# Performance work log

Measured on AMD Instinct MI355X. Metric: run time of the kernel, lower is better.

Reference implementation:

```python
import jax, jax.numpy as jnp
import numpy as np

TOP_K = 8
NUM_EXPERTS = 256
N_GROUP = 8
TOPK_GROUP = 4
SCALE = 2.5
RENORMALIZE = True
TOKENS = 131072


def setup_inputs() -> dict:
    key = jax.random.key(0)
    k1, k2 = jax.random.split(key)
    router_logits = jax.random.normal(k1, (TOKENS, NUM_EXPERTS), dtype=jnp.float32)
    expert_bias = jax.random.normal(k2, (NUM_EXPERTS,), dtype=jnp.float32) * 0.1
    return {"router_logits": router_logits, "expert_bias": expert_bias}


def _group_limited_topk(biased):
    # biased: [T, E]
    T = biased.shape[0]
    epg = NUM_EXPERTS // N_GROUP  # experts per group
    grouped = biased.reshape(T, N_GROUP, epg)
    # group score = sum of top-2 expert scores in each group
    top2_vals, _ = jax.lax.top_k(grouped, 2)
    group_scores = top2_vals.sum(axis=-1)  # [T, G]
    _, group_idx = jax.lax.top_k(group_scores, TOPK_GROUP)  # [T, Kg]
    group_mask = jnp.zeros((T, N_GROUP), dtype=bool).at[
        jnp.arange(T)[:, None], group_idx
    ].set(True)
    score_mask = jnp.repeat(group_mask, epg, axis=-1)  # [T, E]
    masked = jnp.where(score_mask, biased, -jnp.inf)
    _, topk_ids = jax.lax.top_k(masked, TOP_K)  # [T, K]
    return topk_ids


def reference(router_logits, expert_bias):
    scores = jax.nn.sigmoid(router_logits.astype(jnp.float32)).astype(router_logits.dtype)
    topk_ids = _group_limited_topk(scores + expert_bias)
    topk_weights = jnp.take_along_axis(scores, topk_ids, axis=-1)  # [T, K]
    if RENORMALIZE and TOP_K > 1:
        topk_weights = topk_weights / (topk_weights.sum(axis=-1, keepdims=True) + 1e-20)
    topk_weights = topk_weights * SCALE
    return topk_weights, topk_ids
```

## Files before the change

kernel.cpp:

```cpp
#include <hip/hip_runtime.h>
#include <math.h>


#define SWZF(x, mask) __int_as_float(__builtin_amdgcn_ds_swizzle(__float_as_int(x), (((mask) << 10) | 0x1F)))
#define SWZI(x, mask) __builtin_amdgcn_ds_swizzle((x), (((mask) << 10) | 0x1F))

__global__ __launch_bounds__(256) void router_topk_kernel(
    const float* __restrict__ logits,
    const float* __restrict__ bias,
    float* __restrict__ out_w,
    float* __restrict__ out_id,
    int T)
{
    const float NEGINF = -__builtin_inff();
    const int tid = threadIdx.x;
    const int s = tid & 7;
    const int token = blockIdx.x * 32 + (tid >> 3);
    if (token >= T) return;

    const float* row = logits + (size_t)token * 256 + s * 32;
    const float* brw = bias + s * 32;

    float v[8][4];
    int   ix[8][4];

    #pragma unroll
    for (int c = 0; c < 8; ++c) {
        float4 l = ((const float4*)row)[c];
        float4 b = ((const float4*)brw)[c];
        #pragma unroll
        for (int k = 0; k < 4; ++k) {
            float x = (&l.x)[k];
            v[c][k] = 1.0f / (1.0f + expf(-x)) + (&b.x)[k];
            ix[c][k] = s * 32 + c * 4 + k;
        }
    }

    float t1 = NEGINF, t2 = NEGINF;
    #pragma unroll
    for (int c = 0; c < 8; ++c) {
        #pragma unroll
        for (int k = 0; k < 4; ++k) {
            float val = v[c][k];
            t2 = fmaxf(t2, fminf(t1, val));
            t1 = fmaxf(t1, val);
        }
    }
    const float gs = t1 + t2;

    int rank = 0;
    #define RANKSTEP(m, hb) { \
        float gj = SWZF(gs, m); \
        rank += (gj > gs || (gj == gs && (s & (hb)))) ? 1 : 0; }
    RANKSTEP(1, 1) RANKSTEP(2, 2) RANKSTEP(3, 2)
    RANKSTEP(4, 4) RANKSTEP(5, 4) RANKSTEP(6, 4) RANKSTEP(7, 4)
    #undef RANKSTEP
    const bool selected = rank < 4;

    #pragma unroll
    for (int c = 0; c < 8; ++c) {
        #pragma unroll
        for (int k = 0; k < 4; ++k)
            v[c][k] = selected ? v[c][k] : NEGINF;
    }

    #pragma unroll
    for (int c = 0; c < 8; ++c) {
        #define CE(a,b) { \
            bool sw = (v[c][a] < v[c][b]) || (v[c][a] == v[c][b] && ix[c][a] > ix[c][b]); \
            float tv = sw ? v[c][b] : v[c][a]; \
            float uv = sw ? v[c][a] : v[c][b]; \
            int   ti = sw ? ix[c][b] : ix[c][a]; \
            int   ui = sw ? ix[c][a] : ix[c][b]; \
            v[c][a] = tv; v[c][b] = uv; ix[c][a] = ti; ix[c][b] = ui; }
        CE(0,1) CE(2,3) CE(0,2) CE(1,3) CE(1,2)
        #undef CE
    }

    float keepV = 0.0f; int keepI = 0;
    const int sbase8 = s << 3;
    #pragma unroll
    for (int r = 0; r < 8; ++r) {
        #define PICK(av, ai, bv, bi, rv, ri) { \
            bool t = ((bv) > (av)); \
            rv = t ? (bv) : (av); ri = t ? (bi) : (ai); }
        float w0v, w1v, w2v, w3v, x0v, x1v, bv;
        int   w0i, w1i, w2i, w3i, x0i, x1i, bi;
        PICK(v[0][0], ix[0][0], v[1][0], ix[1][0], w0v, w0i)
        PICK(v[2][0], ix[2][0], v[3][0], ix[3][0], w1v, w1i)
        PICK(v[4][0], ix[4][0], v[5][0], ix[5][0], w2v, w2i)
        PICK(v[6][0], ix[6][0], v[7][0], ix[7][0], w3v, w3i)
        PICK(w0v, w0i, w1v, w1i, x0v, x0i)
        PICK(w2v, w2i, w3v, w3i, x1v, x1i)
        PICK(x0v, x0i, x1v, x1i, bv, bi)
        #undef PICK
        #define BFLY(m) { \
            float ov = SWZF(bv, m); int oi = SWZI(bi, m); \
            bool t = (ov > bv) || (ov == bv && oi < bi); \
            bv = t ? ov : bv; bi = t ? oi : bi; }
        BFLY(1) BFLY(2) BFLY(4)
        #undef BFLY
        if (s == r) { keepV = bv; keepI = bi; }
        const int d = (bi >> 2) - sbase8;
        #pragma unroll
        for (int c = 0; c < 8; ++c) {
            bool hit = (d == c);
            v[c][0]  = hit ? v[c][1]  : v[c][0];
            ix[c][0] = hit ? ix[c][1] : ix[c][0];
            v[c][1]  = hit ? v[c][2]  : v[c][1];
            ix[c][1] = hit ? ix[c][2] : ix[c][1];
            v[c][2]  = hit ? v[c][3]  : v[c][2];
            ix[c][2] = hit ? ix[c][3] : ix[c][2];
            v[c][3]  = hit ? NEGINF   : v[c][3];
        }
    }

    float w = keepV - bias[keepI];
    float sum = w;
    sum += SWZF(sum, 1);
    sum += SWZF(sum, 2);
    sum += SWZF(sum, 4);
    w = w / (sum + 1e-20f) * 2.5f;

    out_w[(size_t)token * 8 + s]  = w;
    out_id[(size_t)token * 8 + s] = (float)keepI;
}

extern "C" void kernel_launch(void* const* d_in, const int* in_sizes, int n_in,
                              void* d_out, int out_size, void* d_ws, size_t ws_size,
                              hipStream_t stream) {
    const float* logits = (const float*)d_in[0];
    const float* bias   = (const float*)d_in[1];
    const int E = in_sizes[1];
    const int T = in_sizes[0] / E;
    float* out_w  = (float*)d_out;
    float* out_id = out_w + (size_t)T * 8;
    const int blocks = (T + 31) / 32;
    router_topk_kernel<<<blocks, 256, 0, stream>>>(logits, bias, out_w, out_id, T);
}
```

Before: 210.2 us.

## Use fast approximate sigmoid with margin check and exact-recompute fallback

Computes the sigmoid with hardware exp2 and rcp approximations instead of the exact expf and division, then checks whether the group-selection or top-k decisions sit within small error margins. If any decision is close to a tie, the token is recomputed with the exact sigmoid and reselected. This aims to cut the transcendental arithmetic cost while keeping results identical to the exact path. The cost is an extra ninth selection round plus margin reductions, and divergent fallback work for tokens that trip the check.

```diff
diff --git a/kernel.cpp b/kernel.cpp
--- a/kernel.cpp
+++ b/kernel.cpp
@@ -13,6 +13,8 @@
     int T)
 {
     const float NEGINF = -__builtin_inff();
+    const float EM = 4e-6f;
+    const float GM = 1.2e-5f;
     const int tid = threadIdx.x;
     const int s = tid & 7;
     const int token = blockIdx.x * 32 + (tid >> 3);
@@ -24,95 +26,127 @@
     float v[8][4];
     int   ix[8][4];
 
-    #pragma unroll
-    for (int c = 0; c < 8; ++c) {
-        float4 l = ((const float4*)row)[c];
-        float4 b = ((const float4*)brw)[c];
+    auto compute = [&](int exact) {
         #pragma unroll
-        for (int k = 0; k < 4; ++k) {
-            float x = (&l.x)[k];
-            v[c][k] = 1.0f / (1.0f + expf(-x)) + (&b.x)[k];
-            ix[c][k] = s * 32 + c * 4 + k;
+        for (int c = 0; c < 8; ++c) {
+            float4 l = ((const float4*)row)[c];
+            float4 b = ((const float4*)brw)[c];
+            #pragma unroll
+            for (int k = 0; k < 4; ++k) {
+                float x = (&l.x)[k];
+                float sg;
+                if (exact) {
+                    sg = 1.0f / (1.0f + expf(-x));
+                } else {
+                    float e = __builtin_amdgcn_exp2f(x * -1.4426950408889634f);
+                    sg = __builtin_amdgcn_rcpf(1.0f + e);
+                }
+                v[c][k] = sg + (&b.x)[k];
+            }
         }
-    }
-
-    float t1 = NEGINF, t2 = NEGINF;
-    #pragma unroll
-    for (int c = 0; c < 8; ++c) {
-        #pragma unroll
-        for (int k = 0; k < 4; ++k) {
-            float val = v[c][k];
-            t2 = fmaxf(t2, fminf(t1, val));
-            t1 = fmaxf(t1, val);
-        }
-    }
-    const float gs = t1 + t2;
-
-    int rank = 0;
-    #define RANKSTEP(m, hb) { \
-        float gj = SWZF(gs, m); \
-        rank += (gj > gs || (gj == gs && (s & (hb)))) ? 1 : 0; }
-    RANKSTEP(1, 1) RANKSTEP(2, 2) RANKSTEP(3, 2)
-    RANKSTEP(4, 4) RANKSTEP(5, 4) RANKSTEP(6, 4) RANKSTEP(7, 4)
-    #undef RANKSTEP
-    const bool selected = rank < 4;
-
-    #pragma unroll
-    for (int c = 0; c < 8; ++c) {
-        #pragma unroll
-        for (int k = 0; k < 4; ++k)
-            v[c][k] = selected ? v[c][k] : NEGINF;
-    }
-
-    #pragma unroll
-    for (int c = 0; c < 8; ++c) {
-        #define CE(a,b) { \
-            bool sw = (v[c][a] < v[c][b]) || (v[c][a] == v[c][b] && ix[c][a] > ix[c][b]); \
-            float tv = sw ? v[c][b] : v[c][a]; \
-            float uv = sw ? v[c][a] : v[c][b]; \
-            int   ti = sw ? ix[c][b] : ix[c][a]; \
-            int   ui = sw ? ix[c][a] : ix[c][b]; \
-            v[c][a] = tv; v[c][b] = uv; ix[c][a] = ti; ix[c][b] = ui; }
-        CE(0,1) CE(2,3) CE(0,2) CE(1,3) CE(1,2)
-        #undef CE
-    }
+    };
 
     float keepV = 0.0f; int keepI = 0;
     const int sbase8 = s << 3;
-    #pragma unroll
-    for (int r = 0; r < 8; ++r) {
-        #define PICK(av, ai, bv, bi, rv, ri) { \
-            bool t = ((bv) > (av)); \
-            rv = t ? (bv) : (av); ri = t ? (bi) : (ai); }
-        float w0v, w1v, w2v, w3v, x0v, x1v, bv;
-        int   w0i, w1i, w2i, w3i, x0i, x1i, bi;
-        PICK(v[0][0], ix[0][0], v[1][0], ix[1][0], w0v, w0i)
-        PICK(v[2][0], ix[2][0], v[3][0], ix[3][0], w1v, w1i)
-        PICK(v[4][0], ix[4][0], v[5][0], ix[5][0], w2v, w2i)
-        PICK(v[6][0], ix[6][0], v[7][0], ix[7][0], w3v, w3i)
-        PICK(w0v, w0i, w1v, w1i, x0v, x0i)
-        PICK(w2v, w2i, w3v, w3i, x1v, x1i)
-        PICK(x0v, x0i, x1v, x1i, bv, bi)
-        #undef PICK
-        #define BFLY(m) { \
-            float ov = SWZF(bv, m); int oi = SWZI(bi, m); \
-            bool t = (ov > bv) || (ov == bv && oi < bi); \
-            bv = t ? ov : bv; bi = t ? oi : bi; }
-        BFLY(1) BFLY(2) BFLY(4)
-        #undef BFLY
-        if (s == r) { keepV = bv; keepI = bi; }
-        const int d = (bi >> 2) - sbase8;
+
+    auto select = [&](bool& flag) {
+        #pragma unroll
+        for (int c = 0; c < 8; ++c)
+            #pragma unroll
+            for (int k = 0; k < 4; ++k)
+                ix[c][k] = s * 32 + c * 4 + k;
+
+        float t1 = NEGINF, t2 = NEGINF;
         #pragma unroll
         for (int c = 0; c < 8; ++c) {
-            bool hit = (d == c);
-            v[c][0]  = hit ? v[c][1]  : v[c][0];
-            ix[c][0] = hit ? ix[c][1] : ix[c][0];
-            v[c][1]  = hit ? v[c][2]  : v[c][1];
-            ix[c][1] = hit ? ix[c][2] : ix[c][1];
-            v[c][2]  = hit ? v[c][3]  : v[c][2];
-            ix[c][2] = hit ? ix[c][3] : ix[c][2];
-            v[c][3]  = hit ? NEGINF   : v[c][3];
+            #pragma unroll
+            for (int k = 0; k < 4; ++k) {
+                float val = v[c][k];
+                t2 = fmaxf(t2, fminf(t1, val));
+                t1 = fmaxf(t1, val);
+            }
         }
+        const float gs = t1 + t2;
+
+        int rank = 0;
+        #define RANKSTEP(m, hb) { \
+            float gj = SWZF(gs, m); \
+            rank += (gj > gs || (gj == gs && (s & (hb)))) ? 1 : 0; }
+        RANKSTEP(1, 1) RANKSTEP(2, 2) RANKSTEP(3, 2)
+        RANKSTEP(4, 4) RANKSTEP(5, 4) RANKSTEP(6, 4) RANKSTEP(7, 4)
+        #undef RANKSTEP
+        const bool selected = rank < 4;
+
+        float a  = selected ? NEGINF : gs;
+        float nb = selected ? -gs : NEGINF;
+        a  = fmaxf(a,  SWZF(a, 1));  nb = fmaxf(nb, SWZF(nb, 1));
+        a  = fmaxf(a,  SWZF(a, 2));  nb = fmaxf(nb, SWZF(nb, 2));
+        a  = fmaxf(a,  SWZF(a, 4));  nb = fmaxf(nb, SWZF(nb, 4));
+        flag = ((-nb) - a) < GM;
+
+        #pragma unroll
+        for (int c = 0; c < 8; ++c) {
+            #define CE(x,y) { \
+                bool sw = (v[c][x] < v[c][y]) || (v[c][x] == v[c][y] && ix[c][x] > ix[c][y]); \
+                float tv = sw ? v[c][y] : v[c][x]; \
+                float uv = sw ? v[c][x] : v[c][y]; \
+                int   ti = sw ? ix[c][y] : ix[c][x]; \
+                int   ui = sw ? ix[c][x] : ix[c][y]; \
+                v[c][x] = tv; v[c][y] = uv; ix[c][x] = ti; ix[c][y] = ui; }
+            CE(0,1) CE(2,3) CE(0,2) CE(1,3) CE(1,2)
+            #undef CE
+        }
+
+        float prev = 0.0f;
+        #pragma unroll
+        for (int r = 0; r < 9; ++r) {
+            #define PICK(av, ai, bv_, bi_, rv, ri) { \
+                bool t = ((bv_) > (av)); \
+                rv = t ? (bv_) : (av); ri = t ? (bi_) : (ai); }
+            float w0v, w1v, w2v, w3v, x0v, x1v, bv;
+            int   w0i, w1i, w2i, w3i, x0i, x1i, bi;
+            PICK(v[0][0], ix[0][0], v[1][0], ix[1][0], w0v, w0i)
+            PICK(v[2][0], ix[2][0], v[3][0], ix[3][0], w1v, w1i)
+            PICK(v[4][0], ix[4][0], v[5][0], ix[5][0], w2v, w2i)
+            PICK(v[6][0], ix[6][0], v[7][0], ix[7][0], w3v, w3i)
+            PICK(w0v, w0i, w1v, w1i, x0v, x0i)
+            PICK(w2v, w2i, w3v, w3i, x1v, x1i)
+            PICK(x0v, x0i, x1v, x1i, bv, bi)
+            #undef PICK
+            bv = selected ? bv : NEGINF;
+            #define BFLY(m) { \
+                float ov = SWZF(bv, m); int oi = SWZI(bi, m); \
+                bool t = (ov > bv) || (ov == bv && oi < bi); \
+                bv = t ? ov : bv; bi = t ? oi : bi; }
+            BFLY(1) BFLY(2) BFLY(4)
+            #undef BFLY
+            if (r > 0) flag = flag || ((prev - bv) < EM);
+            prev = bv;
+            if (r < 8) {
+                if (s == r) { keepV = bv; keepI = bi; }
+                const int d = (bi >> 2) - sbase8;
+                #pragma unroll
+                for (int c = 0; c < 8; ++c) {
+                    bool hit = (d == c);
+                    v[c][0]  = hit ? v[c][1]  : v[c][0];
+                    ix[c][0] = hit ? ix[c][1] : ix[c][0];
+                    v[c][1]  = hit ? v[c][2]  : v[c][1];
+                    ix[c][1] = hit ? ix[c][2] : ix[c][1];
+                    v[c][2]  = hit ? v[c][3]  : v[c][2];
+                    ix[c][2] = hit ? ix[c][3] : ix[c][2];
+                    v[c][3]  = hit ? NEGINF   : v[c][3];
+                }
+            }
+        }
+    };
+
+    bool flag;
+    compute(0);
+    select(flag);
+    if (flag) {
+        compute(1);
+        bool f2;
+        select(f2);
     }
 
     float w = keepV - bias[keepI];
```

New measurement: 233.5 us. 11.1% more time.
